# Kernel optimization log

Hardware: AMD Instinct MI355X
Metric: run time of the kernel (lower is better)

The kernel has to match this reference:

```python
import jax, jax.numpy as jnp
import numpy as np
import math

B, L, D, P = 2, 2048, 256, 32
PI = math.pi


def _layernorm(x, g, b, eps=1e-5):
    m = x.mean(-1, keepdims=True)
    v = x.var(-1, keepdims=True)
    return (x - m) / jnp.sqrt(v + eps) * g + b


def setup_inputs() -> dict:
    key = jax.random.key(0)
    ks = jax.random.split(key, 16)
    sd = 1.0 / math.sqrt(D)
    f32 = jnp.float32
    inp = {
        "x": jax.random.normal(ks[0], (B, L, D), f32),
        # key_encoder: Linear(D, P)
        "key_W": jax.random.normal(ks[1], (D, P), f32) * sd,
        "key_b": jnp.zeros((P,), f32),
        # value_encoder: Linear(D, D)
        "val_W": jax.random.normal(ks[2], (D, D), f32) * sd,
        "val_b": jnp.zeros((D,), f32),
        # refiner: LayerNorm(D), Linear(D, 2D), GELU, Linear(2D, D)
        "ln1_g": jnp.ones((D,), f32),
        "ln1_b": jnp.zeros((D,), f32),
        "W1": jax.random.normal(ks[3], (D, 2 * D), f32) * sd,
        "b1": jnp.zeros((2 * D,), f32),
        "W2": jax.random.normal(ks[4], (2 * D, D), f32) * (1.0 / math.sqrt(2 * D)),
        "b2": jnp.zeros((D,), f32),
        # to_out: LayerNorm(D), Linear(D, D)
        "ln2_g": jnp.ones((D,), f32),
        "ln2_b": jnp.zeros((D,), f32),
        "Wo": jax.random.normal(ks[5], (D, D), f32) * sd,
        "bo": jnp.zeros((D,), f32),
    }
    return inp


def reference(x, key_W, key_b, val_W, val_b, ln1_g, ln1_b, W1, b1, W2, b2,
              ln2_g, ln2_b, Wo, bo):
    # key phases in (-pi, pi); phasor exp(i*theta) handled as (cos, sin)
    phases = jnp.tanh(x @ key_W + key_b) * PI          # (B, L, P)
    values = x @ val_W + val_b                          # (B, L, D)

    cos_p = jnp.cos(phases)
    sin_p = jnp.sin(phases)
    # torch.roll(shifts=1, dims=1) then zero the first position -> shift right, row 0 = 0
    zrow = jnp.zeros_like(cos_p[:, :1])
    cos_s = jnp.concatenate([zrow, cos_p[:, :-1]], axis=1)
    sin_s = jnp.concatenate([zrow, sin_p[:, :-1]], axis=1)

    # odd positions hold values
    vmask = (jnp.arange(L) % 2 == 1).astype(x.dtype)    # (L,)
    mv = values * vmask[None, :, None]                  # (B, L, D)

    # bind: outer product phasor (P) x value (D); real/imag parts
    bound_re = cos_s[..., None] * mv[:, :, None, :]     # (B, L, P, D)
    bound_im = sin_s[..., None] * mv[:, :, None, :]
    mem_re = jnp.cumsum(bound_re, axis=1)
    mem_im = jnp.cumsum(bound_im, axis=1)

    # retrieve: Re[ memory * exp(-i*theta) ] summed over phases
    retrieved = (jnp.einsum('blpd,blp->bld', mem_re, cos_p)
                 + jnp.einsum('blpd,blp->bld', mem_im, sin_p))

    valid = jnp.maximum(jnp.cumsum(vmask), 1.0)         # (L,)
    retrieved = retrieved / (jnp.sqrt(valid)[None, :, None] * math.sqrt(P))

    h = _layernorm(retrieved, ln1_g, ln1_b)
    h = jax.nn.gelu(h @ W1 + b1, approximate=False)
    refined = h @ W2 + b2
    out = x + (_layernorm(refined, ln2_g, ln2_b) @ Wo + bo)
    return out
```

## Files before the change

### kernel.cpp

```cpp
#include <hip/hip_runtime.h>
#include <math.h>

#define BB 2
#define LL 2048
#define DD 256
#define PP 32
#define NC 64
#define PI_F 3.14159265358979323846f

typedef __attribute__((ext_vector_type(8))) short bf16x8;
typedef __attribute__((ext_vector_type(4))) float f32x4;
typedef unsigned short ushort_t;
typedef unsigned int uint_t;

__device__ inline ushort_t f2bf(float x) {
    uint_t u = __float_as_uint(x);
    uint_t r = (u + 0x7fffu + ((u >> 16) & 1u)) >> 16;
    return (ushort_t)r;
}

__device__ inline int swzc(int row, int col) {
    return (col & ~63) | ((((col >> 3) & 7) ^ (row & 7)) << 3);
}
__device__ inline int swze(int row, int col) {
    return (col & ~63) | (col & 7) | ((((col >> 3) & 7) ^ (row & 7)) << 3);
}

__global__ __launch_bounds__(256) void prep_key_kernel(
    const float* __restrict__ W1, const float* __restrict__ W2,
    const float* __restrict__ Wo, const float* __restrict__ valW,
    const float* __restrict__ x, const float* __restrict__ key_W,
    const float* __restrict__ key_b,
    ushort_t* __restrict__ W1t, ushort_t* __restrict__ W2t,
    ushort_t* __restrict__ Wot, ushort_t* __restrict__ valWt,
    float2* __restrict__ ph)
{
    const int bid = blockIdx.x;
    const int t = threadIdx.x;
    if (bid < 96) {
        __shared__ float T[64][65];
        const float* W; ushort_t* Wt; int K, N, tile;
        if (bid < 32)      { W = W1;   Wt = W1t;   K = 256; N = 512; tile = bid; }
        else if (bid < 64) { W = W2;   Wt = W2t;   K = 512; N = 256; tile = bid - 32; }
        else if (bid < 80) { W = Wo;   Wt = Wot;   K = 256; N = 256; tile = bid - 64; }
        else               { W = valW; Wt = valWt; K = 256; N = 256; tile = bid - 80; }
        const int ntiles = N / 64;
        const int k0 = (tile / ntiles) * 64, n0 = (tile % ntiles) * 64;
        {
            const int rr = t >> 2, cb = (t & 3) * 16;
            #pragma unroll
            for (int i = 0; i < 16; i += 4) {
                const float4 v = *(const float4*)&W[(k0 + rr) * N + n0 + cb + i];
                T[rr][cb + i + 0] = v.x; T[rr][cb + i + 1] = v.y;
                T[rr][cb + i + 2] = v.z; T[rr][cb + i + 3] = v.w;
            }
        }
        __syncthreads();
        {
            const int n = t >> 2, kb = (t & 3) * 16;
            #pragma unroll
            for (int i = 0; i < 16; ++i)
                Wt[(n0 + n) * K + k0 + kb + i] = f2bf(T[kb + i][n]);
        }
    } else {
        __shared__ ushort_t xt[16][264];
        __shared__ ushort_t kwT[32][264];
        __shared__ float rbuf[4][2][16][17];
        const int row0 = (bid - 96) * 16;
        {
            const int l = t >> 4, cb = (t & 15) * 16;
            const float* src = &x[(long)(row0 + l) * DD + cb];
            ushort_t tmp[16];
            #pragma unroll
            for (int i = 0; i < 4; ++i) {
                const float4 v = *(const float4*)&src[i * 4];
                tmp[i*4+0] = f2bf(v.x); tmp[i*4+1] = f2bf(v.y);
                tmp[i*4+2] = f2bf(v.z); tmp[i*4+3] = f2bf(v.w);
            }
            *(uint4*)&xt[l][cb]     = *(uint4*)&tmp[0];
            *(uint4*)&xt[l][cb + 8] = *(uint4*)&tmp[8];
        }
        {
            #pragma unroll
            for (int i = 0; i < 8; ++i) {
                const int idx4 = i * 256 + t;
                const int k = idx4 >> 3, pc = (idx4 & 7) * 4;
                const float4 v = *(const float4*)&key_W[k * 32 + pc];
                kwT[pc + 0][k] = f2bf(v.x);
                kwT[pc + 1][k] = f2bf(v.y);
                kwT[pc + 2][k] = f2bf(v.z);
                kwT[pc + 3][k] = f2bf(v.w);
            }
        }
        __syncthreads();
        const int wv = t >> 6, lane = t & 63;
        const int qd = lane >> 4, mc = lane & 15;
        f32x4 acc0 = {0.f,0.f,0.f,0.f}, acc1 = {0.f,0.f,0.f,0.f};
        #pragma unroll
        for (int ks = 0; ks < 2; ++ks) {
            const int ko = wv * 64 + ks * 32 + qd * 8;
            const bf16x8 a  = *(const bf16x8*)&xt[mc][ko];
            const bf16x8 b0 = *(const bf16x8*)&kwT[mc][ko];
            const bf16x8 b1 = *(const bf16x8*)&kwT[16 + mc][ko];
            acc0 = __builtin_amdgcn_mfma_f32_16x16x32_bf16(a, b0, acc0, 0, 0, 0);
            acc1 = __builtin_amdgcn_mfma_f32_16x16x32_bf16(a, b1, acc1, 0, 0, 0);
        }
        #pragma unroll
        for (int r = 0; r < 4; ++r) {
            rbuf[wv][0][qd * 4 + r][mc] = acc0[r];
            rbuf[wv][1][qd * 4 + r][mc] = acc1[r];
        }
        __syncthreads();
        #pragma unroll
        for (int rep = 0; rep < 2; ++rep) {
            const int idx = rep * 256 + t;
            const int p = idx & 31, l = idx >> 5;
            const int nf = p >> 4, mcol = p & 15;
            float a = key_b[p] + rbuf[0][nf][l][mcol] + rbuf[1][nf][l][mcol]
                    + rbuf[2][nf][l][mcol] + rbuf[3][nf][l][mcol];
            a = tanhf(a) * PI_F;
            float sn, cs;
            sincosf(a, &sn, &cs);
            ph[(long)(row0 + l) * PP + p] = make_float2(cs, sn);
        }
    }
}

__global__ __launch_bounds__(256) void valbind_kernel(
    const float* __restrict__ x, const float2* __restrict__ ph,
    const ushort_t* __restrict__ valWt, const float* __restrict__ val_b,
    ushort_t* __restrict__ VoddT, float* __restrict__ Mt)
{
    __shared__ ushort_t xsb[16][264];
    __shared__ ushort_t VdT[64][40];
    __shared__ ushort_t phsT[64][40];
    __shared__ float    Ms[64][68];

    const int tid = threadIdx.x;
    const int bid = blockIdx.x;
    const int b  = bid >> 8;
    const int c  = (bid >> 2) & 63;
    const int dq = bid & 3;
    const int base = b * LL;
    const int r0 = 32 * c;

    {
        const int j = tid >> 4, cb = (tid & 15) * 16;
        const float* src = &x[(long)(base + r0 + 2 * j + 1) * DD + cb];
        ushort_t tmp[16];
        #pragma unroll
        for (int i = 0; i < 4; ++i) {
            const float4 v = *(const float4*)&src[i * 4];
            tmp[i*4+0] = f2bf(v.x); tmp[i*4+1] = f2bf(v.y);
            tmp[i*4+2] = f2bf(v.z); tmp[i*4+3] = f2bf(v.w);
        }
        *(uint4*)&xsb[j][cb]     = *(uint4*)&tmp[0];
        *(uint4*)&xsb[j][cb + 8] = *(uint4*)&tmp[8];
    }
    {
        const int j = tid >> 4, qb = (tid & 15) * 4;
        const float4 v = *(const float4*)((const float*)ph +
                              (long)(base + r0 + 2 * j) * 64 + qb);
        phsT[qb + 0][j] = f2bf(v.x);
        phsT[qb + 1][j] = f2bf(v.y);
        phsT[qb + 2][j] = f2bf(v.z);
        phsT[qb + 3][j] = f2bf(v.w);
    }
    for (int e = tid; e < 64 * 16; e += 256) {
        phsT[e >> 4][16 + (e & 15)] = 0;
        VdT[e >> 4][16 + (e & 15)] = 0;
    }
    __syncthreads();

    const int wv = tid >> 6, lane = tid & 63;
    const int qd = lane >> 4, mc = lane & 15;

    f32x4 va = {0.f,0.f,0.f,0.f};
    const int dloc = wv * 16 + mc;
    const int ng = dq * 64 + dloc;
    const ushort_t* B0 = &valWt[(long)ng * 256];
    #pragma unroll
    for (int ks = 0; ks < 8; ++ks) {
        const bf16x8 a  = *(const bf16x8*)&xsb[mc][ks * 32 + qd * 8];
        const bf16x8 b0 = *(const bf16x8*)&B0[ks * 32 + qd * 8];
        va = __builtin_amdgcn_mfma_f32_16x16x32_bf16(a, b0, va, 0, 0, 0);
    }
    {
        const float bb = val_b[ng];
        #pragma unroll
        for (int r = 0; r < 4; ++r)
            VdT[dloc][qd * 4 + r] = f2bf(va[r] + bb);
    }
    __syncthreads();

    const bf16x8 a2 = *(const bf16x8*)&phsT[wv * 16 + mc][qd * 8];
    f32x4 macc[4];
    #pragma unroll
    for (int nf = 0; nf < 4; ++nf) {
        f32x4 z = {0.f,0.f,0.f,0.f};
        const bf16x8 b2 = *(const bf16x8*)&VdT[nf * 16 + mc][qd * 8];
        macc[nf] = __builtin_amdgcn_mfma_f32_16x16x32_bf16(a2, b2, z, 0, 0, 0);
    }
    #pragma unroll
    for (int nf = 0; nf < 4; ++nf) {
        #pragma unroll
        for (int r = 0; r < 4; ++r)
            Ms[nf * 16 + mc][wv * 16 + qd * 4 + r] = macc[nf][r];
    }
    __syncthreads();

    {
        float* dst = &Mt[((long)(b * NC + c) * 256 + dq * 64) * 64];
        #pragma unroll
        for (int p = 0; p < 4; ++p) {
            const int idx4 = p * 256 + tid;
            const int dl = idx4 >> 4, q4 = (idx4 & 15) * 4;
            *(float4*)&dst[dl * 64 + q4] = *(const float4*)&Ms[dl][q4];
        }
    }
    if (tid < 64) {
        ushort_t* vd = &VoddT[((long)(b * NC + c) * 256 + dq * 64 + tid) * 16];
        *(uint4*)&vd[0] = *(const uint4*)&VdT[tid][0];
        *(uint4*)&vd[8] = *(const uint4*)&VdT[tid][8];
    }
}

__global__ __launch_bounds__(256) void prefix_kernel(
    const float* __restrict__ M, ushort_t* __restrict__ Mpre_b)
{
    __shared__ float segsum[4][64];
    const int tid = threadIdx.x;
    const int b  = blockIdx.x >> 8;
    const int cg = blockIdx.x & 255;
    const int col = cg * 64 + (tid & 63);
    const int seg = tid >> 6;
    const long base = (long)b * NC * 16384 + col;

    float v[16], s = 0.f;
    #pragma unroll
    for (int i = 0; i < 16; ++i) {
        v[i] = M[base + (long)(seg * 16 + i) * 16384];
        s += v[i];
    }
    segsum[seg][tid & 63] = s;
    __syncthreads();
    float run = 0.f;
    #pragma unroll
    for (int sg = 0; sg < 3; ++sg)
        if (sg < seg) run += segsum[sg][tid & 63];
    #pragma unroll
    for (int i = 0; i < 16; ++i) {
        const long a = base + (long)(seg * 16 + i) * 16384;
        Mpre_b[a] = f2bf(run);
        run += v[i];
    }
}

__global__ __launch_bounds__(512) void retrieve_mlp_kernel(
    const float* __restrict__ ph, const ushort_t* __restrict__ Mpre_b,
    const ushort_t* __restrict__ VoddT,
    const float* __restrict__ ln1_g, const float* __restrict__ ln1_b,
    const ushort_t* __restrict__ W1t, const float* __restrict__ b1,
    const ushort_t* __restrict__ W2t, const float* __restrict__ b2,
    const float* __restrict__ ln2_g, const float* __restrict__ ln2_b,
    const ushort_t* __restrict__ Wot, const float* __restrict__ bo,
    const float* __restrict__ x, float* __restrict__ out)
{
    __shared__ ushort_t Bs_m[256][64];
    __shared__ ushort_t Bs_v[256][32];
    __shared__ ushort_t As_ph[16][64];
    __shared__ ushort_t Bs_sh[16][64];
    __shared__ ushort_t As_p[16][40];
    __shared__ float    refct[16][264];
    __shared__ ushort_t rhat_s[16][256];
    __shared__ ushort_t h_s[16][512];
    __shared__ ushort_t shT[16][256];

    const int tid = threadIdx.x;
    const int b = blockIdx.x >> 7;
    const int c = (blockIdx.x >> 1) & 63;
    const int h = blockIdx.x & 1;
    const int l0g = 32 * c + 16 * h;
    const long rowbase = (long)b * LL + l0g;

    {
        const ushort_t* src = &Mpre_b[(long)(b * NC + c) * 16384];
        #pragma unroll
        for (int p = 0; p < 4; ++p) {
            const int idx8 = p * 512 + tid;
            const int d = idx8 >> 3, ch = idx8 & 7;
            *(uint4*)&Bs_m[d][8 * (ch ^ (d & 7))] = *(const uint4*)&src[idx8 * 8];
        }
    }
    if (tid < 256) {
        const int r = tid >> 4, q4 = (tid & 15) * 4;
        const int c4 = swze(r, q4);
        const float4 vv = *(const float4*)((const float*)ph + (rowbase + r) * 64 + q4);
        ushort_t t0[4] = {f2bf(vv.x), f2bf(vv.y), f2bf(vv.z), f2bf(vv.w)};
        *(uint2*)&As_ph[r][c4] = *(uint2*)t0;
        const float4 w = *(const float4*)((const float*)ph +
                             ((long)b * LL + 32 * c + 2 * r) * 64 + q4);
        ushort_t t1[4] = {f2bf(w.x), f2bf(w.y), f2bf(w.z), f2bf(w.w)};
        *(uint2*)&Bs_sh[r][c4] = *(uint2*)t1;
    }
    {
        const ushort_t* src = &VoddT[(long)(b * NC + c) * 4096];
        const int rw = tid >> 1, cch = tid & 1;
        *(uint4*)&Bs_v[rw][8 * (cch ^ (rw & 3))] = *(const uint4*)&src[tid * 8];
        *(uint4*)&Bs_v[rw][8 * ((2 + cch) ^ (rw & 3))] = make_uint4(0, 0, 0, 0);
        if (tid < 256) As_p[tid >> 4][16 + (tid & 15)] = 0;
    }
    __syncthreads();

    const int wv = tid >> 6, lane = tid & 63;
    const int qd = lane >> 4, mc = lane & 15;
    const int sk = (tid & 7) * 8, srow = tid >> 3;
    const int wch = 8 * ((tid & 7) ^ (srow & 7));
    const int m7 = mc & 7;

    {
        f32x4 sacc = {0.f, 0.f, 0.f, 0.f};
        #pragma unroll
        for (int ks = 0; ks < 2; ++ks) {
            const int lc = 8 * ((ks * 4 + qd) ^ m7);
            const bf16x8 a  = *(const bf16x8*)&As_ph[mc][lc];
            const bf16x8 bb = *(const bf16x8*)&Bs_sh[mc][lc];
            sacc = __builtin_amdgcn_mfma_f32_16x16x32_bf16(a, bb, sacc, 0, 0, 0);
        }
        if (wv == 0) {
            #pragma unroll
            for (int r = 0; r < 4; ++r) {
                const int l = qd * 4 + r;
                As_p[l][mc] = (2 * mc + 1 <= 16 * h + l) ? f2bf(sacc[r])
                                                         : (ushort_t)0;
            }
        }
    }

    f32x4 acc[2];
    #pragma unroll
    for (int i = 0; i < 2; ++i) acc[i] = (f32x4){0.f, 0.f, 0.f, 0.f};
    #pragma unroll
    for (int i = 0; i < 2; ++i) {
        const int d0 = wv * 32 + i * 16;
        #pragma unroll
        for (int ks = 0; ks < 2; ++ks) {
            const int lc = 8 * ((ks * 4 + qd) ^ m7);
            const bf16x8 a  = *(const bf16x8*)&As_ph[mc][lc];
            const bf16x8 bb = *(const bf16x8*)&Bs_m[d0 + mc][lc];
            acc[i] = __builtin_amdgcn_mfma_f32_16x16x32_bf16(a, bb, acc[i], 0, 0, 0);
        }
    }
    __syncthreads();

    {
        const bf16x8 a2 = *(const bf16x8*)&As_p[mc][qd * 8];
        #pragma unroll
        for (int i = 0; i < 2; ++i) {
            const int d0 = wv * 32 + i * 16;
            const bf16x8 b2 = *(const bf16x8*)&Bs_v[d0 + mc][8 * (qd ^ (mc & 3))];
            acc[i] = __builtin_amdgcn_mfma_f32_16x16x32_bf16(a2, b2, acc[i], 0, 0, 0);
        }
    }

    #pragma unroll
    for (int r = 0; r < 4; ++r) {
        const int l = qd * 4 + r;
        int va = (l0g + l + 1) >> 1; if (va < 1) va = 1;
        const float sc = 0.17677669529663687f * rsqrtf((float)va);
        #pragma unroll
        for (int i = 0; i < 2; ++i)
            refct[l][wv * 32 + i * 16 + mc] = acc[i][r] * sc;
    }
    __syncthreads();

    {
        const int row = tid >> 5, cg = (tid & 31) * 8;
        float s = 0.f, sq = 0.f;
        #pragma unroll
        for (int i = 0; i < 8; ++i) {
            const float v = refct[row][cg + i];
            s += v; sq += v * v;
        }
        s += __shfl_xor(s, 1, 32);  sq += __shfl_xor(sq, 1, 32);
        s += __shfl_xor(s, 2, 32);  sq += __shfl_xor(sq, 2, 32);
        s += __shfl_xor(s, 4, 32);  sq += __shfl_xor(sq, 4, 32);
        s += __shfl_xor(s, 8, 32);  sq += __shfl_xor(sq, 8, 32);
        s += __shfl_xor(s, 16, 32); sq += __shfl_xor(sq, 16, 32);
        const float m = s * (1.f / 256.f);
        const float inv = rsqrtf(sq * (1.f / 256.f) - m * m + 1e-5f);
        ushort_t o16[8];
        #pragma unroll
        for (int i = 0; i < 8; ++i) {
            const int cc = cg + i;
            o16[i] = f2bf((refct[row][cc] - m) * inv * ln1_g[cc] + ln1_b[cc]);
        }
        *(uint4*)&rhat_s[row][swzc(row, cg)] = *(uint4*)&o16[0];
    }

    #pragma unroll
    for (int nh = 0; nh < 2; ++nh) {
        f32x4 acc1[2];
        acc1[0] = (f32x4){0.f,0.f,0.f,0.f};
        acc1[1] = (f32x4){0.f,0.f,0.f,0.f};
        for (int k0 = 0; k0 < 256; k0 += 64) {
            __syncthreads();
            #pragma unroll
            for (int rr = 0; rr < 4; ++rr) {
                const int n = rr * 64 + srow;
                *(uint4*)&Bs_m[n][wch] =
                    *(const uint4*)&W1t[(long)(nh * 256 + n) * 256 + k0 + sk];
            }
            __syncthreads();
            #pragma unroll
            for (int ks = 0; ks < 2; ++ks) {
                const int lc = 8 * ((ks * 4 + qd) ^ m7);
                const bf16x8 a = *(const bf16x8*)&rhat_s[mc][k0 + lc];
                #pragma unroll
                for (int nf = 0; nf < 2; ++nf) {
                    const bf16x8 bb = *(const bf16x8*)&Bs_m[wv * 32 + nf * 16 + mc][lc];
                    acc1[nf] = __builtin_amdgcn_mfma_f32_16x16x32_bf16(a, bb, acc1[nf], 0, 0, 0);
                }
            }
        }
        #pragma unroll
        for (int nf = 0; nf < 2; ++nf) {
            const int n = nh * 256 + wv * 32 + nf * 16 + mc;
            const float bb = b1[n];
            #pragma unroll
            for (int r = 0; r < 4; ++r) {
                float v = acc1[nf][r] + bb;
                v = 0.5f * v * (1.f + erff(v * 0.70710678118654752f));
                const int rw = qd * 4 + r;
                h_s[rw][swze(rw, n)] = f2bf(v);
            }
        }
    }

    f32x4 acc2[2];
    acc2[0] = (f32x4){0.f,0.f,0.f,0.f};
    acc2[1] = (f32x4){0.f,0.f,0.f,0.f};
    for (int k0 = 0; k0 < 512; k0 += 64) {
        __syncthreads();
        #pragma unroll
        for (int rr = 0; rr < 4; ++rr) {
            const int n = rr * 64 + srow;
            *(uint4*)&Bs_m[n][wch] = *(const uint4*)&W2t[(long)n * 512 + k0 + sk];
        }
        __syncthreads();
        #pragma unroll
        for (int ks = 0; ks < 2; ++ks) {
            const int lc = 8 * ((ks * 4 + qd) ^ m7);
            const bf16x8 a = *(const bf16x8*)&h_s[mc][k0 + lc];
            #pragma unroll
            for (int nf = 0; nf < 2; ++nf) {
                const bf16x8 bb = *(const bf16x8*)&Bs_m[wv * 32 + nf * 16 + mc][lc];
                acc2[nf] = __builtin_amdgcn_mfma_f32_16x16x32_bf16(a, bb, acc2[nf], 0, 0, 0);
            }
        }
    }
    #pragma unroll
    for (int nf = 0; nf < 2; ++nf) {
        const int n = wv * 32 + nf * 16 + mc;
        const float bb = b2[n];
        #pragma unroll
        for (int r = 0; r < 4; ++r)
            refct[qd * 4 + r][n] = acc2[nf][r] + bb;
    }
    __syncthreads();

    {
        const int row = tid >> 5, cg = (tid & 31) * 8;
        float s = 0.f, sq = 0.f;
        #pragma unroll
        for (int i = 0; i < 8; ++i) {
            const float v = refct[row][cg + i];
            s += v; sq += v * v;
        }
        s += __shfl_xor(s, 1, 32);  sq += __shfl_xor(sq, 1, 32);
        s += __shfl_xor(s, 2, 32);  sq += __shfl_xor(sq, 2, 32);
        s += __shfl_xor(s, 4, 32);  sq += __shfl_xor(sq, 4, 32);
        s += __shfl_xor(s, 8, 32);  sq += __shfl_xor(sq, 8, 32);
        s += __shfl_xor(s, 16, 32); sq += __shfl_xor(sq, 16, 32);
        const float m = s * (1.f / 256.f);
        const float inv = rsqrtf(sq * (1.f / 256.f) - m * m + 1e-5f);
        ushort_t o16[8];
        #pragma unroll
        for (int i = 0; i < 8; ++i) {
            const int cc = cg + i;
            o16[i] = f2bf((refct[row][cc] - m) * inv * ln2_g[cc] + ln2_b[cc]);
        }
        *(uint4*)&shT[row][swzc(row, cg)] = *(uint4*)&o16[0];
    }

    f32x4 acc3[2];
    acc3[0] = (f32x4){0.f,0.f,0.f,0.f};
    acc3[1] = (f32x4){0.f,0.f,0.f,0.f};
    for (int k0 = 0; k0 < 256; k0 += 64) {
        __syncthreads();
        #pragma unroll
        for (int rr = 0; rr < 4; ++rr) {
            const int n = rr * 64 + srow;
            *(uint4*)&Bs_m[n][wch] = *(const uint4*)&Wot[(long)n * 256 + k0 + sk];
        }
        __syncthreads();
        #pragma unroll
        for (int ks = 0; ks < 2; ++ks) {
            const int lc = 8 * ((ks * 4 + qd) ^ m7);
            const bf16x8 a = *(const bf16x8*)&shT[mc][k0 + lc];
            #pragma unroll
            for (int nf = 0; nf < 2; ++nf) {
                const bf16x8 bb = *(const bf16x8*)&Bs_m[wv * 32 + nf * 16 + mc][lc];
                acc3[nf] = __builtin_amdgcn_mfma_f32_16x16x32_bf16(a, bb, acc3[nf], 0, 0, 0);
            }
        }
    }
    #pragma unroll
    for (int nf = 0; nf < 2; ++nf) {
        const int n = wv * 32 + nf * 16 + mc;
        const float bb = bo[n];
        #pragma unroll
        for (int r = 0; r < 4; ++r) {
            const long row = rowbase + qd * 4 + r;
            out[row * DD + n] = acc3[nf][r] + bb + x[row * DD + n];
        }
    }
}

extern "C" void kernel_launch(void* const* d_in, const int* in_sizes, int n_in,
                              void* d_out, int out_size, void* d_ws, size_t ws_size,
                              hipStream_t stream)
{
    const float* x     = (const float*)d_in[0];
    const float* key_W = (const float*)d_in[1];
    const float* key_b = (const float*)d_in[2];
    const float* val_W = (const float*)d_in[3];
    const float* val_b = (const float*)d_in[4];
    const float* ln1_g = (const float*)d_in[5];
    const float* ln1_b = (const float*)d_in[6];
    const float* W1    = (const float*)d_in[7];
    const float* b1    = (const float*)d_in[8];
    const float* W2    = (const float*)d_in[9];
    const float* b2    = (const float*)d_in[10];
    const float* ln2_g = (const float*)d_in[11];
    const float* ln2_b = (const float*)d_in[12];
    const float* Wo    = (const float*)d_in[13];
    const float* bo    = (const float*)d_in[14];
    float* outp = (float*)d_out;

    float* ws = (float*)d_ws;
    float*  ph      = ws;
    float*  Mt      = ws + 262144;
    ushort_t* Mpre_b = (ushort_t*)(Mt + 2097152);
    ushort_t* VoddT  = Mpre_b + 2097152;
    ushort_t* rhat_b = VoddT + 524288;
    ushort_t* W1t   = rhat_b + 1048576;
    ushort_t* W2t   = W1t + 131072;
    ushort_t* Wot   = W2t + 131072;
    ushort_t* valWt = Wot + 65536;

    prep_key_kernel<<<352, 256, 0, stream>>>(W1, W2, Wo, val_W, x, key_W, key_b,
                                             W1t, W2t, Wot, valWt, (float2*)ph);
    valbind_kernel<<<512, 256, 0, stream>>>(x, (const float2*)ph, valWt, val_b,
                                            VoddT, Mt);
    prefix_kernel<<<512, 256, 0, stream>>>(Mt, Mpre_b);
    retrieve_mlp_kernel<<<256, 512, 0, stream>>>(ph, Mpre_b, VoddT, ln1_g, ln1_b,
                                                 W1t, b1, W2t, b2, ln2_g, ln2_b,
                                                 Wot, bo, x, outp);
}
```

Before: 120.7 us.

## Load MFMA B operands directly from global memory instead of LDS staging

Drops the shared-memory staging buffer for the memory chunk and for the W1, W2 and Wo weight tiles. Each lane now reads its bf16x8 B fragments straight from global memory (served by L2/L1), which removes the per-k-tile __syncthreads pairs and the LDS writes, and shrinks LDS use so occupancy can rise. The cost is uncoalesced, row-strided global loads per lane and more load latency exposed to the MFMAs, relying on cache hits for the weights shared across blocks.

```diff
diff --git a/kernel.cpp b/kernel.cpp
--- a/kernel.cpp
+++ b/kernel.cpp
@@ -266,7 +266,6 @@
     const ushort_t* __restrict__ Wot, const float* __restrict__ bo,
     const float* __restrict__ x, float* __restrict__ out)
 {
-    __shared__ ushort_t Bs_m[256][64];
     __shared__ ushort_t Bs_v[256][32];
     __shared__ ushort_t As_ph[16][64];
     __shared__ ushort_t Bs_sh[16][64];
@@ -283,15 +282,6 @@
     const int l0g = 32 * c + 16 * h;
     const long rowbase = (long)b * LL + l0g;
 
-    {
-        const ushort_t* src = &Mpre_b[(long)(b * NC + c) * 16384];
-        #pragma unroll
-        for (int p = 0; p < 4; ++p) {
-            const int idx8 = p * 512 + tid;
-            const int d = idx8 >> 3, ch = idx8 & 7;
-            *(uint4*)&Bs_m[d][8 * (ch ^ (d & 7))] = *(const uint4*)&src[idx8 * 8];
-        }
-    }
     if (tid < 256) {
         const int r = tid >> 4, q4 = (tid & 15) * 4;
         const int c4 = swze(r, q4);
@@ -314,8 +304,6 @@
 
     const int wv = tid >> 6, lane = tid & 63;
     const int qd = lane >> 4, mc = lane & 15;
-    const int sk = (tid & 7) * 8, srow = tid >> 3;
-    const int wch = 8 * ((tid & 7) ^ (srow & 7));
     const int m7 = mc & 7;
 
     {
@@ -337,6 +325,7 @@
         }
     }
 
+    const ushort_t* msrc = &Mpre_b[(long)(b * NC + c) * 16384];
     f32x4 acc[2];
     #pragma unroll
     for (int i = 0; i < 2; ++i) acc[i] = (f32x4){0.f, 0.f, 0.f, 0.f};
@@ -347,7 +336,7 @@
         for (int ks = 0; ks < 2; ++ks) {
             const int lc = 8 * ((ks * 4 + qd) ^ m7);
             const bf16x8 a  = *(const bf16x8*)&As_ph[mc][lc];
-            const bf16x8 bb = *(const bf16x8*)&Bs_m[d0 + mc][lc];
+            const bf16x8 bb = *(const bf16x8*)&msrc[(long)(d0 + mc) * 64 + ks * 32 + qd * 8];
             acc[i] = __builtin_amdgcn_mfma_f32_16x16x32_bf16(a, bb, acc[i], 0, 0, 0);
         }
     }
@@ -397,30 +386,26 @@
         }
         *(uint4*)&rhat_s[row][swzc(row, cg)] = *(uint4*)&o16[0];
     }
+    __syncthreads();
 
     #pragma unroll
     for (int nh = 0; nh < 2; ++nh) {
         f32x4 acc1[2];
         acc1[0] = (f32x4){0.f,0.f,0.f,0.f};
         acc1[1] = (f32x4){0.f,0.f,0.f,0.f};
+        const long nb0 = (long)(nh * 256 + wv * 32 + mc) * 256;
+        const long nb1 = (long)(nh * 256 + wv * 32 + 16 + mc) * 256;
+        #pragma unroll
         for (int k0 = 0; k0 < 256; k0 += 64) {
-            __syncthreads();
-            #pragma unroll
-            for (int rr = 0; rr < 4; ++rr) {
-                const int n = rr * 64 + srow;
-                *(uint4*)&Bs_m[n][wch] =
-                    *(const uint4*)&W1t[(long)(nh * 256 + n) * 256 + k0 + sk];
-            }
-            __syncthreads();
             #pragma unroll
             for (int ks = 0; ks < 2; ++ks) {
+                const int kk = k0 + ks * 32 + qd * 8;
                 const int lc = 8 * ((ks * 4 + qd) ^ m7);
-                const bf16x8 a = *(const bf16x8*)&rhat_s[mc][k0 + lc];
-                #pragma unroll
-                for (int nf = 0; nf < 2; ++nf) {
-                    const bf16x8 bb = *(const bf16x8*)&Bs_m[wv * 32 + nf * 16 + mc][lc];
-                    acc1[nf] = __builtin_amdgcn_mfma_f32_16x16x32_bf16(a, bb, acc1[nf], 0, 0, 0);
-                }
+                const bf16x8 a  = *(const bf16x8*)&rhat_s[mc][k0 + lc];
+                const bf16x8 b0 = *(const bf16x8*)&W1t[nb0 + kk];
+                const bf16x8 b1v = *(const bf16x8*)&W1t[nb1 + kk];
+                acc1[0] = __builtin_amdgcn_mfma_f32_16x16x32_bf16(a, b0, acc1[0], 0, 0, 0);
+                acc1[1] = __builtin_amdgcn_mfma_f32_16x16x32_bf16(a, b1v, acc1[1], 0, 0, 0);
             }
         }
         #pragma unroll
@@ -436,26 +421,25 @@
             }
         }
     }
+    __syncthreads();
 
     f32x4 acc2[2];
     acc2[0] = (f32x4){0.f,0.f,0.f,0.f};
     acc2[1] = (f32x4){0.f,0.f,0.f,0.f};
-    for (int k0 = 0; k0 < 512; k0 += 64) {
-        __syncthreads();
-        #pragma unroll
-        for (int rr = 0; rr < 4; ++rr) {
-            const int n = rr * 64 + srow;
-            *(uint4*)&Bs_m[n][wch] = *(const uint4*)&W2t[(long)n * 512 + k0 + sk];
-        }
-        __syncthreads();
-        #pragma unroll
-        for (int ks = 0; ks < 2; ++ks) {
-            const int lc = 8 * ((ks * 4 + qd) ^ m7);
-            const bf16x8 a = *(const bf16x8*)&h_s[mc][k0 + lc];
-            #pragma unroll
-            for (int nf = 0; nf < 2; ++nf) {
-                const bf16x8 bb = *(const bf16x8*)&Bs_m[wv * 32 + nf * 16 + mc][lc];
-                acc2[nf] = __builtin_amdgcn_mfma_f32_16x16x32_bf16(a, bb, acc2[nf], 0, 0, 0);
+    {
+        const long nb0 = (long)(wv * 32 + mc) * 512;
+        const long nb1 = (long)(wv * 32 + 16 + mc) * 512;
+        #pragma unroll
+        for (int k0 = 0; k0 < 512; k0 += 64) {
+            #pragma unroll
+            for (int ks = 0; ks < 2; ++ks) {
+                const int kk = k0 + ks * 32 + qd * 8;
+                const int lc = 8 * ((ks * 4 + qd) ^ m7);
+                const bf16x8 a  = *(const bf16x8*)&h_s[mc][k0 + lc];
+                const bf16x8 b0 = *(const bf16x8*)&W2t[nb0 + kk];
+                const bf16x8 b1v = *(const bf16x8*)&W2t[nb1 + kk];
+                acc2[0] = __builtin_amdgcn_mfma_f32_16x16x32_bf16(a, b0, acc2[0], 0, 0, 0);
+                acc2[1] = __builtin_amdgcn_mfma_f32_16x16x32_bf16(a, b1v, acc2[1], 0, 0, 0);
             }
         }
     }
@@ -492,26 +476,25 @@
         }
         *(uint4*)&shT[row][swzc(row, cg)] = *(uint4*)&o16[0];
     }
+    __syncthreads();
 
     f32x4 acc3[2];
     acc3[0] = (f32x4){0.f,0.f,0.f,0.f};
     acc3[1] = (f32x4){0.f,0.f,0.f,0.f};
-    for (int k0 = 0; k0 < 256; k0 += 64) {
-        __syncthreads();
-        #pragma unroll
-        for (int rr = 0; rr < 4; ++rr) {
-            const int n = rr * 64 + srow;
-            *(uint4*)&Bs_m[n][wch] = *(const uint4*)&Wot[(long)n * 256 + k0 + sk];
-        }
-        __syncthreads();
-        #pragma unroll
-        for (int ks = 0; ks < 2; ++ks) {
-            const int lc = 8 * ((ks * 4 + qd) ^ m7);
-            const bf16x8 a = *(const bf16x8*)&shT[mc][k0 + lc];
-            #pragma unroll
-            for (int nf = 0; nf < 2; ++nf) {
-                const bf16x8 bb = *(const bf16x8*)&Bs_m[wv * 32 + nf * 16 + mc][lc];
-                acc3[nf] = __builtin_amdgcn_mfma_f32_16x16x32_bf16(a, bb, acc3[nf], 0, 0, 0);
+    {
+        const long nb0 = (long)(wv * 32 + mc) * 256;
+        const long nb1 = (long)(wv * 32 + 16 + mc) * 256;
+        #pragma unroll
+        for (int k0 = 0; k0 < 256; k0 += 64) {
+            #pragma unroll
+            for (int ks = 0; ks < 2; ++ks) {
+                const int kk = k0 + ks * 32 + qd * 8;
+                const int lc = 8 * ((ks * 4 + qd) ^ m7);
+                const bf16x8 a  = *(const bf16x8*)&shT[mc][k0 + lc];
+                const bf16x8 b0 = *(const bf16x8*)&Wot[nb0 + kk];
+                const bf16x8 b1v = *(const bf16x8*)&Wot[nb1 + kk];
+                acc3[0] = __builtin_amdgcn_mfma_f32_16x16x32_bf16(a, b0, acc3[0], 0, 0, 0);
+                acc3[1] = __builtin_amdgcn_mfma_f32_16x16x32_bf16(a, b1v, acc3[1], 0, 0, 0);
             }
         }
     }
```

Result: slower. 124.2 us (+2.9%).

## Use per-wave private weight tiles with register prefetch to drop block barriers

Applied to the files above, without the earlier changes.

The shared Bs_m buffer becomes per-wave Wbuf slices. Each wave now loads only the 32 weight rows it consumes, so the two block-wide __syncthreads per K-step in the W1/W2/Wo GEMM loops go away. The next weight tile is prefetched into registers while the current tile is used, and the prefetch chains across GEMM stages (W1 into W2 into Wo). This aims to hide global-load latency and barrier stalls, at the cost of more registers. The write-then-read of each wave's own LDS slice relies on intra-wave ordering without an explicit wave barrier.

```diff
diff --git a/kernel.cpp b/kernel.cpp
--- a/kernel.cpp
+++ b/kernel.cpp
@@ -266,7 +266,7 @@
     const ushort_t* __restrict__ Wot, const float* __restrict__ bo,
     const float* __restrict__ x, float* __restrict__ out)
 {
-    __shared__ ushort_t Bs_m[256][64];
+    __shared__ ushort_t Wbuf[8][32][64];
     __shared__ ushort_t Bs_v[256][32];
     __shared__ ushort_t As_ph[16][64];
     __shared__ ushort_t Bs_sh[16][64];
@@ -283,15 +283,18 @@
     const int l0g = 32 * c + 16 * h;
     const long rowbase = (long)b * LL + l0g;
 
-    {
-        const ushort_t* src = &Mpre_b[(long)(b * NC + c) * 16384];
-        #pragma unroll
-        for (int p = 0; p < 4; ++p) {
-            const int idx8 = p * 512 + tid;
-            const int d = idx8 >> 3, ch = idx8 & 7;
-            *(uint4*)&Bs_m[d][8 * (ch ^ (d & 7))] = *(const uint4*)&src[idx8 * 8];
-        }
-    }
+    const int wv = tid >> 6, lane = tid & 63;
+    const int qd = lane >> 4, mc = lane & 15;
+    const int m7 = mc & 7;
+    const int ch = lane & 7, rl8 = lane >> 3;
+    const int wcol = 8 * (ch ^ rl8);
+
+    const ushort_t* msrc = &Mpre_b[(long)(b * NC + c) * 16384];
+    uint4 pre[4];
+    #pragma unroll
+    for (int p = 0; p < 4; ++p)
+        pre[p] = *(const uint4*)&msrc[(wv * 32 + p * 8 + rl8) * 64 + ch * 8];
+
     if (tid < 256) {
         const int r = tid >> 4, q4 = (tid & 15) * 4;
         const int c4 = swze(r, q4);
@@ -310,13 +313,10 @@
         *(uint4*)&Bs_v[rw][8 * ((2 + cch) ^ (rw & 3))] = make_uint4(0, 0, 0, 0);
         if (tid < 256) As_p[tid >> 4][16 + (tid & 15)] = 0;
     }
-    __syncthreads();
-
-    const int wv = tid >> 6, lane = tid & 63;
-    const int qd = lane >> 4, mc = lane & 15;
-    const int sk = (tid & 7) * 8, srow = tid >> 3;
-    const int wch = 8 * ((tid & 7) ^ (srow & 7));
-    const int m7 = mc & 7;
+    #pragma unroll
+    for (int p = 0; p < 4; ++p)
+        *(uint4*)&Wbuf[wv][p * 8 + rl8][wcol] = pre[p];
+    __syncthreads();
 
     {
         f32x4 sacc = {0.f, 0.f, 0.f, 0.f};
@@ -342,12 +342,11 @@
     for (int i = 0; i < 2; ++i) acc[i] = (f32x4){0.f, 0.f, 0.f, 0.f};
     #pragma unroll
     for (int i = 0; i < 2; ++i) {
-        const int d0 = wv * 32 + i * 16;
         #pragma unroll
         for (int ks = 0; ks < 2; ++ks) {
             const int lc = 8 * ((ks * 4 + qd) ^ m7);
             const bf16x8 a  = *(const bf16x8*)&As_ph[mc][lc];
-            const bf16x8 bb = *(const bf16x8*)&Bs_m[d0 + mc][lc];
+            const bf16x8 bb = *(const bf16x8*)&Wbuf[wv][i * 16 + mc][lc];
             acc[i] = __builtin_amdgcn_mfma_f32_16x16x32_bf16(a, bb, acc[i], 0, 0, 0);
         }
     }
@@ -373,6 +372,10 @@
             refct[l][wv * 32 + i * 16 + mc] = acc[i][r] * sc;
     }
     __syncthreads();
+
+    #pragma unroll
+    for (int p = 0; p < 4; ++p)
+        pre[p] = *(const uint4*)&W1t[(long)(wv * 32 + p * 8 + rl8) * 256 + ch * 8];
 
     {
         const int row = tid >> 5, cg = (tid & 31) * 8;
@@ -397,64 +400,83 @@
         }
         *(uint4*)&rhat_s[row][swzc(row, cg)] = *(uint4*)&o16[0];
     }
-
-    #pragma unroll
-    for (int nh = 0; nh < 2; ++nh) {
+    __syncthreads();
+
+    {
         f32x4 acc1[2];
         acc1[0] = (f32x4){0.f,0.f,0.f,0.f};
         acc1[1] = (f32x4){0.f,0.f,0.f,0.f};
-        for (int k0 = 0; k0 < 256; k0 += 64) {
-            __syncthreads();
-            #pragma unroll
-            for (int rr = 0; rr < 4; ++rr) {
-                const int n = rr * 64 + srow;
-                *(uint4*)&Bs_m[n][wch] =
-                    *(const uint4*)&W1t[(long)(nh * 256 + n) * 256 + k0 + sk];
-            }
-            __syncthreads();
+        #pragma unroll
+        for (int t = 0; t < 8; ++t) {
+            const int k0 = (t & 3) * 64;
+            #pragma unroll
+            for (int p = 0; p < 4; ++p)
+                *(uint4*)&Wbuf[wv][p * 8 + rl8][wcol] = pre[p];
+            if (t < 7) {
+                const int nhn = (t + 1) >> 2, k0n = ((t + 1) & 3) * 64;
+                #pragma unroll
+                for (int p = 0; p < 4; ++p)
+                    pre[p] = *(const uint4*)&W1t[(long)(nhn * 256 + wv * 32 + p * 8 + rl8) * 256 + k0n + ch * 8];
+            } else {
+                #pragma unroll
+                for (int p = 0; p < 4; ++p)
+                    pre[p] = *(const uint4*)&W2t[(long)(wv * 32 + p * 8 + rl8) * 512 + ch * 8];
+            }
             #pragma unroll
             for (int ks = 0; ks < 2; ++ks) {
                 const int lc = 8 * ((ks * 4 + qd) ^ m7);
                 const bf16x8 a = *(const bf16x8*)&rhat_s[mc][k0 + lc];
                 #pragma unroll
                 for (int nf = 0; nf < 2; ++nf) {
-                    const bf16x8 bb = *(const bf16x8*)&Bs_m[wv * 32 + nf * 16 + mc][lc];
+                    const bf16x8 bb = *(const bf16x8*)&Wbuf[wv][nf * 16 + mc][lc];
                     acc1[nf] = __builtin_amdgcn_mfma_f32_16x16x32_bf16(a, bb, acc1[nf], 0, 0, 0);
                 }
             }
-        }
-        #pragma unroll
-        for (int nf = 0; nf < 2; ++nf) {
-            const int n = nh * 256 + wv * 32 + nf * 16 + mc;
-            const float bb = b1[n];
-            #pragma unroll
-            for (int r = 0; r < 4; ++r) {
-                float v = acc1[nf][r] + bb;
-                v = 0.5f * v * (1.f + erff(v * 0.70710678118654752f));
-                const int rw = qd * 4 + r;
-                h_s[rw][swze(rw, n)] = f2bf(v);
-            }
-        }
-    }
+            if ((t & 3) == 3) {
+                const int nh = t >> 2;
+                #pragma unroll
+                for (int nf = 0; nf < 2; ++nf) {
+                    const int n = nh * 256 + wv * 32 + nf * 16 + mc;
+                    const float bb = b1[n];
+                    #pragma unroll
+                    for (int r = 0; r < 4; ++r) {
+                        float v = acc1[nf][r] + bb;
+                        v = 0.5f * v * (1.f + erff(v * 0.70710678118654752f));
+                        const int rw = qd * 4 + r;
+                        h_s[rw][swze(rw, n)] = f2bf(v);
+                    }
+                    acc1[nf] = (f32x4){0.f,0.f,0.f,0.f};
+                }
+            }
+        }
+    }
+    __syncthreads();
 
     f32x4 acc2[2];
     acc2[0] = (f32x4){0.f,0.f,0.f,0.f};
     acc2[1] = (f32x4){0.f,0.f,0.f,0.f};
-    for (int k0 = 0; k0 < 512; k0 += 64) {
-        __syncthreads();
-        #pragma unroll
-        for (int rr = 0; rr < 4; ++rr) {
-            const int n = rr * 64 + srow;
-            *(uint4*)&Bs_m[n][wch] = *(const uint4*)&W2t[(long)n * 512 + k0 + sk];
-        }
-        __syncthreads();
+    #pragma unroll
+    for (int it = 0; it < 8; ++it) {
+        const int k0 = it * 64;
+        #pragma unroll
+        for (int p = 0; p < 4; ++p)
+            *(uint4*)&Wbuf[wv][p * 8 + rl8][wcol] = pre[p];
+        if (it < 7) {
+            #pragma unroll
+            for (int p = 0; p < 4; ++p)
+                pre[p] = *(const uint4*)&W2t[(long)(wv * 32 + p * 8 + rl8) * 512 + k0 + 64 + ch * 8];
+        } else {
+            #pragma unroll
+            for (int p = 0; p < 4; ++p)
+                pre[p] = *(const uint4*)&Wot[(long)(wv * 32 + p * 8 + rl8) * 256 + ch * 8];
+        }
         #pragma unroll
         for (int ks = 0; ks < 2; ++ks) {
             const int lc = 8 * ((ks * 4 + qd) ^ m7);
             const bf16x8 a = *(const bf16x8*)&h_s[mc][k0 + lc];
             #pragma unroll
             for (int nf = 0; nf < 2; ++nf) {
-                const bf16x8 bb = *(const bf16x8*)&Bs_m[wv * 32 + nf * 16 + mc][lc];
+                const bf16x8 bb = *(const bf16x8*)&Wbuf[wv][nf * 16 + mc][lc];
                 acc2[nf] = __builtin_amdgcn_mfma_f32_16x16x32_bf16(a, bb, acc2[nf], 0, 0, 0);
             }
         }
@@ -492,25 +514,29 @@
         }
         *(uint4*)&shT[row][swzc(row, cg)] = *(uint4*)&o16[0];
     }
+    __syncthreads();
 
     f32x4 acc3[2];
     acc3[0] = (f32x4){0.f,0.f,0.f,0.f};
     acc3[1] = (f32x4){0.f,0.f,0.f,0.f};
-    for (int k0 = 0; k0 < 256; k0 += 64) {
-        __syncthreads();
-        #pragma unroll
-        for (int rr = 0; rr < 4; ++rr) {
-            const int n = rr * 64 + srow;
-            *(uint4*)&Bs_m[n][wch] = *(const uint4*)&Wot[(long)n * 256 + k0 + sk];
-        }
-        __syncthreads();
+    #pragma unroll
+    for (int it = 0; it < 4; ++it) {
+        const int k0 = it * 64;
+        #pragma unroll
+        for (int p = 0; p < 4; ++p)
+            *(uint4*)&Wbuf[wv][p * 8 + rl8][wcol] = pre[p];
+        if (it < 3) {
+            #pragma unroll
+            for (int p = 0; p < 4; ++p)
+                pre[p] = *(const uint4*)&Wot[(long)(wv * 32 + p * 8 + rl8) * 256 + k0 + 64 + ch * 8];
+        }
         #pragma unroll
         for (int ks = 0; ks < 2; ++ks) {
             const int lc = 8 * ((ks * 4 + qd) ^ m7);
             const bf16x8 a = *(const bf16x8*)&shT[mc][k0 + lc];
             #pragma unroll
             for (int nf = 0; nf < 2; ++nf) {
-                const bf16x8 bb = *(const bf16x8*)&Bs_m[wv * 32 + nf * 16 + mc][lc];
+                const bf16x8 bb = *(const bf16x8*)&Wbuf[wv][nf * 16 + mc][lc];
                 acc3[nf] = __builtin_amdgcn_mfma_f32_16x16x32_bf16(a, bb, acc3[nf], 0, 0, 0);
             }
         }
```

New measurement: 142.9 us. 18.4% more time.
